# Optimization experiments

Hardware: AMD Instinct MI355X
Metric: run time of the kernel (lower is better)

The kernel has to match this reference:

```python
import jax, jax.numpy as jnp
import numpy as np

N = 50000      # nodes
E = 1_600_000  # edges
DIN, HID, OUT, H = 128, 32, 32, 4


def _glorot(key, shape):
    fan_in, fan_out = shape[0], shape[1] if len(shape) > 1 else shape[0]
    s = jnp.sqrt(6.0 / (fan_in + fan_out)).astype(jnp.float32)
    return jax.random.uniform(key, shape, jnp.float32, -s, s)


def setup_inputs() -> dict:
    key = jax.random.key(0)
    ks = jax.random.split(key, 16)
    inp = {
        "x": jax.random.normal(ks[0], (N, DIN), jnp.float32),
        "edge_index": jax.random.randint(ks[1], (2, E), 0, N, dtype=jnp.int32),
        "edge_weight": jax.random.uniform(ks[2], (E, 1), jnp.float32),
        # layer 1: in=DIN, heads=H, out=HID, concat=True
        "Wl1": _glorot(ks[3], (DIN, H * HID)),
        "Wr1": _glorot(ks[4], (DIN, H * HID)),
        "We1": _glorot(ks[5], (1, H * HID)),
        "att1": _glorot(ks[6], (H, HID)),
        "b1": jnp.zeros((H * HID,), jnp.float32),
        # layer 2: in=H*HID, heads=H, out=OUT, concat=False (mean over heads)
        "Wl2": _glorot(ks[7], (H * HID, H * OUT)),
        "Wr2": _glorot(ks[8], (H * HID, H * OUT)),
        "We2": _glorot(ks[9], (1, H * OUT)),
        "att2": _glorot(ks[10], (H, OUT)),
        "b2": jnp.zeros((OUT,), jnp.float32),
    }
    return inp


def gatv2_layer(x, edge_index, edge_weight, Wl, Wr, We, att, b, concat):
    """Faithful PyG GATv2Conv (share_weights=False, negative_slope=0.2,
    add_self_loops=True with fill_value='mean' for edge_attr)."""
    n = x.shape[0]
    heads, c = att.shape
    src, dst = edge_index[0], edge_index[1]
    # add self loops with mean edge weight (PyG default when edge_dim is set)
    loop = jnp.arange(n, dtype=edge_index.dtype)
    src = jnp.concatenate([src, loop])
    dst = jnp.concatenate([dst, loop])
    ew = jnp.concatenate(
        [edge_weight, jnp.full((n, edge_weight.shape[1]), jnp.mean(edge_weight), edge_weight.dtype)], axis=0)

    xl = (x @ Wl).reshape(n, heads, c)   # source transform (lin_l)
    xr = (x @ Wr).reshape(n, heads, c)   # target transform (lin_r)
    e_feat = (ew @ We).reshape(-1, heads, c)

    z = jax.nn.leaky_relu(xl[src] + xr[dst] + e_feat, 0.2)   # [E', H, C]
    logits = jnp.einsum('ehc,hc->eh', z, att)                # [E', H]

    # segment softmax over incoming edges of each target node
    m = jax.ops.segment_max(logits, dst, num_segments=n)
    m = jnp.where(jnp.isfinite(m), m, 0.0)
    p = jnp.exp(logits - m[dst])
    denom = jax.ops.segment_sum(p, dst, num_segments=n)
    alpha = p / (denom[dst] + 1e-16)                          # [E', H]

    out = jax.ops.segment_sum(xl[src] * alpha[..., None], dst, num_segments=n)  # [N, H, C]
    out = out.reshape(n, heads * c) if concat else out.mean(axis=1)
    return out + b


def reference(x, edge_index, edge_weight, Wl1, Wr1, We1, att1, b1,
              Wl2, Wr2, We2, att2, b2):
    h = gatv2_layer(x, edge_index, edge_weight, Wl1, Wr1, We1, att1, b1, concat=True)
    h = jax.nn.elu(h)
    out = gatv2_layer(h, edge_index, edge_weight, Wl2, Wr2, We2, att2, b2, concat=False)
    return out
```

## Files before the change

kernel.cpp:

```cpp
#include <hip/hip_runtime.h>
#include <hip/hip_fp16.h>
#include <math.h>


typedef _Float16 half8 __attribute__((ext_vector_type(8)));
typedef float floatx4 __attribute__((ext_vector_type(4)));

__global__ __launch_bounds__(256) void bucket_hist_sum(
    const int* __restrict__ dst, const float* __restrict__ ew,
    int* __restrict__ bcnt, float* __restrict__ sumbuf, int E) {
    __shared__ int h[256];
    h[threadIdx.x] = 0;
    __syncthreads();
    float s = 0.f;
    for (int i = blockIdx.x * blockDim.x + threadIdx.x; i < E; i += gridDim.x * blockDim.x) {
        atomicAdd(&h[dst[i] >> 8], 1);
        s += ew[i];
    }
#pragma unroll
    for (int off = 1; off <= 32; off <<= 1)
        s += __shfl_xor(s, off, 64);
    if ((threadIdx.x & 63) == 0)
        atomicAdd(sumbuf, s);
    __syncthreads();
    int v = h[threadIdx.x];
    if (v) atomicAdd(&bcnt[threadIdx.x], v);
}

__global__ void bucket_scan(const int* __restrict__ bcnt, int* __restrict__ bbase,
                            int* __restrict__ bcur, int NBK) {
    __shared__ int sh[256];
    int t = threadIdx.x;
    int v = (t < NBK) ? bcnt[t] : 0;
    sh[t] = v;
    __syncthreads();
    for (int off = 1; off < 256; off <<= 1) {
        int y = 0;
        if (t >= off) y = sh[t - off];
        __syncthreads();
        sh[t] += y;
        __syncthreads();
    }
    int ex = sh[t] - v;
    if (t <= NBK) bbase[t] = ex;
    if (t < NBK) bcur[t] = ex;
}

__global__ __launch_bounds__(256) void partition_kernel(
    const int* __restrict__ src, const int* __restrict__ dst, const float* __restrict__ ew,
    int* __restrict__ bcur, int2* __restrict__ srec, int E) {
    __shared__ int h[256];
    __shared__ int gb[256];
    const int t = threadIdx.x;
    h[t] = 0;
    __syncthreads();
    const int base = blockIdx.x * 4096;
    int d[16], sv[16];
    float wv[16];
#pragma unroll
    for (int j = 0; j < 16; j++) {
        int i = base + t + j * 256;
        if (i < E) {
            d[j] = dst[i];
            sv[j] = src[i];
            wv[j] = ew[i];
            atomicAdd(&h[d[j] >> 8], 1);
        } else {
            d[j] = -1;
        }
    }
    __syncthreads();
    int cntt = h[t];
    if (cntt) gb[t] = atomicAdd(&bcur[t], cntt);
    h[t] = 0;
    __syncthreads();
#pragma unroll
    for (int j = 0; j < 16; j++) {
        if (d[j] >= 0) {
            int b = d[j] >> 8;
            int r = atomicAdd(&h[b], 1);
            int pos = gb[b] + r;
            srec[pos] = make_int2(sv[j] | ((d[j] & 255) << 20), __float_as_int(wv[j]));
        }
    }
}

__global__ __launch_bounds__(256) void dst_hist_kernel(
    const int2* __restrict__ srec, const int* __restrict__ bbase,
    int* __restrict__ cnt, int N) {
    __shared__ int h[256];
    const int t = threadIdx.x;
    const int b = blockIdx.x;
    h[t] = 0;
    __syncthreads();
    const int e0 = bbase[b], e1 = bbase[b + 1];
    for (int i = e0 + t; i < e1; i += 256)
        atomicAdd(&h[(srec[i].x >> 20) & 255], 1);
    __syncthreads();
    int node = (b << 8) + t;
    if (node < N) cnt[node] = h[t];
}

__global__ void scan1_kernel(const int* __restrict__ cnt, int* __restrict__ rowp,
                             int* __restrict__ bsum, int N) {
    __shared__ int sh[256];
    int i = blockIdx.x * 256 + threadIdx.x;
    int v = (i < N) ? (cnt[i] + 1) : 0;
    sh[threadIdx.x] = v;
    __syncthreads();
    for (int off = 1; off < 256; off <<= 1) {
        int y = 0;
        if ((int)threadIdx.x >= off) y = sh[threadIdx.x - off];
        __syncthreads();
        sh[threadIdx.x] += y;
        __syncthreads();
    }
    int incl = sh[threadIdx.x];
    if (i < N) rowp[i] = incl - v;
    if (threadIdx.x == 255) bsum[blockIdx.x] = incl;
}

__global__ void scan2_kernel(int* __restrict__ bsum, int nb) {
    __shared__ int sh[256];
    int v = ((int)threadIdx.x < nb) ? bsum[threadIdx.x] : 0;
    sh[threadIdx.x] = v;
    __syncthreads();
    for (int off = 1; off < 256; off <<= 1) {
        int y = 0;
        if ((int)threadIdx.x >= off) y = sh[threadIdx.x - off];
        __syncthreads();
        sh[threadIdx.x] += y;
        __syncthreads();
    }
    int incl = sh[threadIdx.x];
    if ((int)threadIdx.x < nb) bsum[threadIdx.x] = incl - v;
}

__global__ void scan3_kernel(int* __restrict__ rowp, const int* __restrict__ bsum,
                             const int* __restrict__ cnt, const float* __restrict__ sumbuf,
                             int2* __restrict__ crec, int N, int E) {
    int i = blockIdx.x * 256 + threadIdx.x;
    if (i < N) {
        int rp = rowp[i] + bsum[blockIdx.x];
        rowp[i] = rp;
        crec[rp + cnt[i]] = make_int2(i, __float_as_int(sumbuf[0] * (1.0f / (float)E)));
    }
    if (i == 0) rowp[N] = E + N;
}

__global__ __launch_bounds__(256) void refine_kernel(
    const int2* __restrict__ srec, const int* __restrict__ bbase,
    const int* __restrict__ rowp, int2* __restrict__ crec, int N) {
    __shared__ int cur[256];
    const int t = threadIdx.x;
    const int b = blockIdx.x;
    int node = (b << 8) + t;
    cur[t] = (node < N) ? rowp[node] : 0;
    __syncthreads();
    const int e0 = bbase[b], e1 = bbase[b + 1];
    for (int i = e0 + t; i < e1; i += 256) {
        int2 rec = srec[i];
        int dlow = (rec.x >> 20) & 255;
        int pos = atomicAdd(&cur[dlow], 1);
        crec[pos] = make_int2(rec.x & 0xFFFFF, rec.y);
    }
}

__global__ __launch_bounds__(256) void prep_w_kernel(
    const float* __restrict__ Wa, const float* __restrict__ Wb,
    _Float16* __restrict__ Wh) {
    int tid = blockIdx.x * 256 + threadIdx.x;
    int j = tid & 7;
    int lane = (tid >> 3) & 63;
    int f = tid >> 9;
    int kk = f & 3;
    int ct = f >> 2;
    int col = ct * 16 + (lane & 15);
    int k = kk * 32 + ((lane >> 4) << 3) + j;
    float v = (col < 128) ? Wa[k * 128 + col] : Wb[k * 128 + (col - 128)];
    Wh[tid] = (_Float16)v;
}

__global__ __launch_bounds__(256) void gemm_mfma_kernel(
    const float* __restrict__ X, const _Float16* __restrict__ Wh,
    __half* __restrict__ Yh, float* __restrict__ Yb, int N) {
    __shared__ _Float16 Xs[64 * 128];
    const int tid = threadIdx.x;
    const int lane = tid & 63;
    const int w = tid >> 6;
    const int rb = blockIdx.x * 64;

    half8 wf[4][4];
#pragma unroll
    for (int ct = 0; ct < 4; ct++)
#pragma unroll
        for (int kk = 0; kk < 4; kk++)
            wf[ct][kk] = *(const half8*)(Wh + (size_t)(((w * 4 + ct) * 4 + kk) * 512 + lane * 8));

#pragma unroll
    for (int it = 0; it < 8; it++) {
        int c = it * 256 + tid;
        int row = c >> 5;
        int f4 = c & 31;
        float4 v = make_float4(0.f, 0.f, 0.f, 0.f);
        if (rb + row < N)
            v = ((const float4*)X)[(size_t)(rb + row) * 32 + f4];
        _Float16 h[4] = {(_Float16)v.x, (_Float16)v.y, (_Float16)v.z, (_Float16)v.w};
        int byteoff = row * 256 + ((f4 * 8) ^ ((row & 7) << 4));
        *(uint2*)((char*)Xs + byteoff) = *(uint2*)h;
    }
    __syncthreads();

    floatx4 acc[4][4];
#pragma unroll
    for (int ct = 0; ct < 4; ct++)
#pragma unroll
        for (int rt = 0; rt < 4; rt++)
            acc[ct][rt] = (floatx4){0.f, 0.f, 0.f, 0.f};

#pragma unroll
    for (int kk = 0; kk < 4; kk++) {
        half8 xf[4];
#pragma unroll
        for (int rt = 0; rt < 4; rt++) {
            int row = rt * 16 + (lane & 15);
            int kb = kk * 64 + ((lane >> 4) << 4);
            int off = row * 256 + (kb ^ ((row & 7) << 4));
            xf[rt] = *(const half8*)((const char*)Xs + off);
        }
#pragma unroll
        for (int ct = 0; ct < 4; ct++)
#pragma unroll
            for (int rt = 0; rt < 4; rt++)
                acc[ct][rt] = __builtin_amdgcn_mfma_f32_16x16x32_f16(
                    wf[ct][kk], xf[rt], acc[ct][rt], 0, 0, 0);
    }

    const int rsub = lane & 15;
    const int c4 = (lane >> 4) << 2;
#pragma unroll
    for (int ct = 0; ct < 4; ct++) {
        int gct = w * 4 + ct;
#pragma unroll
        for (int rt = 0; rt < 4; rt++) {
            int row = rb + rt * 16 + rsub;
            if (row < N) {
                floatx4 a = acc[ct][rt];
                if (gct < 8) {
                    int col = gct * 16 + c4;
                    __half2 hp[2];
                    hp[0] = __floats2half2_rn(a[0], a[1]);
                    hp[1] = __floats2half2_rn(a[2], a[3]);
                    *(uint2*)(Yh + (size_t)row * 128 + col) = *(uint2*)hp;
                } else {
                    int col = (gct - 8) * 16 + c4;
                    *(float4*)(Yb + (size_t)row * 128 + col) =
                        make_float4(a[0], a[1], a[2], a[3]);
                }
            }
        }
    }
}

template <int CTRL>
__device__ __forceinline__ float dpp_sum_step(float v) {
    int t = __builtin_amdgcn_update_dpp(0, __float_as_int(v), CTRL, 0xF, 0xF, true);
    return v + __int_as_float(t);
}

__device__ __forceinline__ float2 cvt_h2(unsigned u) {
    __half2 h = *(__half2*)&u;
    return __half22float2(h);
}

__global__ __launch_bounds__(256) void agg_kernel(
    const __half* __restrict__ xlh, const float* __restrict__ xr,
    const int* __restrict__ rowp, const int2* __restrict__ crec,
    const float* __restrict__ We, const float* __restrict__ att, const float* __restrict__ bias,
    float* __restrict__ out, int N, int mode) {
    const int wid = threadIdx.x >> 6;
    const int lane = threadIdx.x & 63;
    const int n = blockIdx.x * 4 + wid;
    if (n >= N) return;
    const int g = lane >> 4;
    const int q = lane & 15;
    const int c0 = q << 3;
    const float LOG2E = 1.4426950408889634f;

    float we[8], xv[8], at6[8], at4[8];
    {
        float4 wA = *(const float4*)(We + c0);
        float4 wB = *(const float4*)(We + c0 + 4);
        we[0]=wA.x; we[1]=wA.y; we[2]=wA.z; we[3]=wA.w;
        we[4]=wB.x; we[5]=wB.y; we[6]=wB.z; we[7]=wB.w;
        float4 rA = *(const float4*)(xr + (size_t)n * 128 + c0);
        float4 rB = *(const float4*)(xr + (size_t)n * 128 + c0 + 4);
        xv[0]=rA.x; xv[1]=rA.y; xv[2]=rA.z; xv[3]=rA.w;
        xv[4]=rB.x; xv[5]=rB.y; xv[6]=rB.z; xv[7]=rB.w;
        float4 aA = *(const float4*)(att + c0);
        float4 aB = *(const float4*)(att + c0 + 4);
        float av[8] = {aA.x, aA.y, aA.z, aA.w, aB.x, aB.y, aB.z, aB.w};
#pragma unroll
        for (int c = 0; c < 8; c++) {
            at6[c] = 0.6f * LOG2E * av[c];
            at4[c] = 0.4f * LOG2E * av[c];
        }
    }

    float acc[8];
#pragma unroll
    for (int c = 0; c < 8; c++) acc[c] = 0.f;
    float l0 = 0.f;

    const int e0 = __builtin_amdgcn_readfirstlane(rowp[n]);
    const int e1 = __builtin_amdgcn_readfirstlane(rowp[n + 1]);
    const int cnt = e1 - e0;
    const int T = (cnt + 3) >> 2;

    auto recload = [&](int i) -> int2 {
        int idx = e0 + (i << 2) + g;
        idx = (idx < e1 - 1) ? idx : (e1 - 1);
        return crec[idx];
    };
    auto gatherx = [&](int s) -> int4 {
        return *(const int4*)(xlh + (size_t)s * 128 + c0);
    };
    auto process = [&](int4 xh, float w, bool valid) {
        float2 x01 = cvt_h2(xh.x), x23 = cvt_h2(xh.y);
        float2 x45 = cvt_h2(xh.z), x67 = cvt_h2(xh.w);
        float xs[8] = {x01.x, x01.y, x23.x, x23.y, x45.x, x45.y, x67.x, x67.y};
        float p = 0.f;
#pragma unroll
        for (int c = 0; c < 8; c++) {
            float z = xs[c] + fmaf(w, we[c], xv[c]);
            p = fmaf(at6[c], z, fmaf(at4[c], fabsf(z), p));
        }
        p = dpp_sum_step<0xB1>(p);
        p = dpp_sum_step<0x4E>(p);
        float qe = valid ? __builtin_amdgcn_exp2f(p) : 0.f;
        l0 += qe;
#pragma unroll
        for (int c = 0; c < 8; c++) acc[c] = fmaf(qe, xs[c], acc[c]);
    };

    int2 r0 = recload(0), r1 = recload(1), r2 = recload(2), r3 = recload(3);
    int4 x0 = gatherx(r0.x), x1 = gatherx(r1.x);
    for (int i = 0; i < T; ++i) {
        int2 r4 = recload(i + 4);
        int4 x2 = gatherx(r2.x);
        process(x0, __int_as_float(r0.y), (e0 + (i << 2) + g) < e1);
        r0 = r1; r1 = r2; r2 = r3; r3 = r4;
        x0 = x1; x1 = x2;
    }

    l0 += __shfl_xor(l0, 16, 64);
    l0 += __shfl_xor(l0, 32, 64);
#pragma unroll
    for (int c = 0; c < 8; c++) {
        acc[c] += __shfl_xor(acc[c], 16, 64);
        acc[c] += __shfl_xor(acc[c], 32, 64);
    }
    float rdenom = 1.0f / (l0 + 1e-16f);
    float r[8];
#pragma unroll
    for (int c = 0; c < 8; c++) r[c] = acc[c] * rdenom;

    if (mode == 0) {
        if (g == 0) {
            float4 bA = *(const float4*)(bias + c0);
            float4 bB = *(const float4*)(bias + c0 + 4);
            float bv[8] = {bA.x, bA.y, bA.z, bA.w, bB.x, bB.y, bB.z, bB.w};
            float o[8];
#pragma unroll
            for (int c = 0; c < 8; c++) {
                float v = r[c] + bv[c];
                o[c] = (v > 0.f) ? v : (__expf(v) - 1.f);
            }
            float* op = out + (size_t)n * 128 + c0;
            *(float4*)op       = make_float4(o[0], o[1], o[2], o[3]);
            *(float4*)(op + 4) = make_float4(o[4], o[5], o[6], o[7]);
        }
    } else {
#pragma unroll
        for (int c = 0; c < 8; c++) {
            r[c] += __shfl_xor(r[c], 4, 64);
            r[c] += __shfl_xor(r[c], 8, 64);
        }
        if (lane < 4) {
            int w0 = lane << 3;
            float4 bA = *(const float4*)(bias + w0);
            float4 bB = *(const float4*)(bias + w0 + 4);
            float bv[8] = {bA.x, bA.y, bA.z, bA.w, bB.x, bB.y, bB.z, bB.w};
            float o[8];
#pragma unroll
            for (int c = 0; c < 8; c++) o[c] = 0.25f * r[c] + bv[c];
            float* op = out + (size_t)n * 32 + w0;
            *(float4*)op       = make_float4(o[0], o[1], o[2], o[3]);
            *(float4*)(op + 4) = make_float4(o[4], o[5], o[6], o[7]);
        }
    }
}

extern "C" void kernel_launch(void* const* d_in, const int* in_sizes, int n_in,
                              void* d_out, int out_size, void* d_ws, size_t ws_size,
                              hipStream_t stream) {
    const float* x    = (const float*)d_in[0];
    const int*  eidx  = (const int*)d_in[1];
    const float* ew   = (const float*)d_in[2];
    const float* Wl1  = (const float*)d_in[3];
    const float* Wr1  = (const float*)d_in[4];
    const float* We1  = (const float*)d_in[5];
    const float* att1 = (const float*)d_in[6];
    const float* b1   = (const float*)d_in[7];
    const float* Wl2  = (const float*)d_in[8];
    const float* Wr2  = (const float*)d_in[9];
    const float* We2  = (const float*)d_in[10];
    const float* att2 = (const float*)d_in[11];
    const float* b2   = (const float*)d_in[12];

    const int N = in_sizes[0] / 128;
    const int E = in_sizes[1] / 2;
    const int* src = eidx;
    const int* dst = eidx + E;
    const int NBK = (N + 255) >> 8;

    char* p = (char*)d_ws;
    auto alloc = [&](size_t bytes) -> void* {
        void* r = (void*)p;
        p += (bytes + 255) & ~(size_t)255;
        return r;
    };
    __half* xlh   = (__half*)alloc((size_t)N * 128 * sizeof(__half));
    float* xr     = (float*)alloc((size_t)N * 128 * sizeof(float));
    float* h1     = (float*)alloc((size_t)N * 128 * sizeof(float));
    int2*  crec   = (int2*)alloc((size_t)(E + N) * sizeof(int2));
    int*   rowp   = (int*)alloc((size_t)(N + 1) * sizeof(int));
    int*   cnt    = (int*)alloc((size_t)N * sizeof(int));
    int*   bcnt   = (int*)alloc(260 * sizeof(int));
    float* sumbuf = (float*)(bcnt + 256);
    int*   bbase  = (int*)alloc(260 * sizeof(int));
    int*   bcur   = (int*)alloc(260 * sizeof(int));
    int*   bsum   = (int*)alloc(256 * sizeof(int));
    _Float16* Wh1 = (_Float16*)alloc(32768 * sizeof(_Float16));
    _Float16* Wh2 = (_Float16*)alloc(32768 * sizeof(_Float16));
    int2*  srec   = (int2*)h1;

    hipMemsetAsync(bcnt, 0, 260 * sizeof(int), stream);

    prep_w_kernel<<<128, 256, 0, stream>>>(Wl1, Wr1, Wh1);
    prep_w_kernel<<<128, 256, 0, stream>>>(Wl2, Wr2, Wh2);

    bucket_hist_sum<<<1024, 256, 0, stream>>>(dst, ew, bcnt, sumbuf, E);
    bucket_scan<<<1, 256, 0, stream>>>(bcnt, bbase, bcur, NBK);
    partition_kernel<<<(E + 4095) / 4096, 256, 0, stream>>>(src, dst, ew, bcur, srec, E);
    dst_hist_kernel<<<NBK, 256, 0, stream>>>(srec, bbase, cnt, N);

    int nb = (N + 255) / 256;
    scan1_kernel<<<nb, 256, 0, stream>>>(cnt, rowp, bsum, N);
    scan2_kernel<<<1, 256, 0, stream>>>(bsum, nb);
    scan3_kernel<<<nb, 256, 0, stream>>>(rowp, bsum, cnt, sumbuf, crec, N, E);

    refine_kernel<<<NBK, 256, 0, stream>>>(srec, bbase, rowp, crec, N);

    gemm_mfma_kernel<<<(N + 63) / 64, 256, 0, stream>>>(x, Wh1, xlh, xr, N);
    agg_kernel<<<(N + 3) / 4, 256, 0, stream>>>(xlh, xr, rowp, crec,
                                                We1, att1, b1, h1, N, 0);
    gemm_mfma_kernel<<<(N + 63) / 64, 256, 0, stream>>>(h1, Wh2, xlh, xr, N);
    agg_kernel<<<(N + 3) / 4, 256, 0, stream>>>(xlh, xr, rowp, crec,
                                                We2, att2, b2, (float*)d_out, N, 1);
}
```

Before: 377.6 us.

## Replace two-pass bucket partition CSR build with direct global-atomic histogram and scatter

After: 499.8 us. 1.32x slower.

```diff
diff --git a/kernel.cpp b/kernel.cpp
--- a/kernel.cpp
+++ b/kernel.cpp
@@ -6,15 +6,12 @@
 typedef _Float16 half8 __attribute__((ext_vector_type(8)));
 typedef float floatx4 __attribute__((ext_vector_type(4)));
 
-__global__ __launch_bounds__(256) void bucket_hist_sum(
+__global__ __launch_bounds__(256) void hist_sum_kernel(
     const int* __restrict__ dst, const float* __restrict__ ew,
-    int* __restrict__ bcnt, float* __restrict__ sumbuf, int E) {
-    __shared__ int h[256];
-    h[threadIdx.x] = 0;
-    __syncthreads();
+    int* __restrict__ cnt, float* __restrict__ sumbuf, int E) {
     float s = 0.f;
-    for (int i = blockIdx.x * blockDim.x + threadIdx.x; i < E; i += gridDim.x * blockDim.x) {
-        atomicAdd(&h[dst[i] >> 8], 1);
+    for (int i = blockIdx.x * 256 + threadIdx.x; i < E; i += gridDim.x * 256) {
+        atomicAdd(&cnt[dst[i]], 1);
         s += ew[i];
     }
 #pragma unroll
@@ -22,83 +19,6 @@
         s += __shfl_xor(s, off, 64);
     if ((threadIdx.x & 63) == 0)
         atomicAdd(sumbuf, s);
-    __syncthreads();
-    int v = h[threadIdx.x];
-    if (v) atomicAdd(&bcnt[threadIdx.x], v);
-}
-
-__global__ void bucket_scan(const int* __restrict__ bcnt, int* __restrict__ bbase,
-                            int* __restrict__ bcur, int NBK) {
-    __shared__ int sh[256];
-    int t = threadIdx.x;
-    int v = (t < NBK) ? bcnt[t] : 0;
-    sh[t] = v;
-    __syncthreads();
-    for (int off = 1; off < 256; off <<= 1) {
-        int y = 0;
-        if (t >= off) y = sh[t - off];
-        __syncthreads();
-        sh[t] += y;
-        __syncthreads();
-    }
-    int ex = sh[t] - v;
-    if (t <= NBK) bbase[t] = ex;
-    if (t < NBK) bcur[t] = ex;
-}
-
-__global__ __launch_bounds__(256) void partition_kernel(
-    const int* __restrict__ src, const int* __restrict__ dst, const float* __restrict__ ew,
-    int* __restrict__ bcur, int2* __restrict__ srec, int E) {
-    __shared__ int h[256];
-    __shared__ int gb[256];
-    const int t = threadIdx.x;
-    h[t] = 0;
-    __syncthreads();
-    const int base = blockIdx.x * 4096;
-    int d[16], sv[16];
-    float wv[16];
-#pragma unroll
-    for (int j = 0; j < 16; j++) {
-        int i = base + t + j * 256;
-        if (i < E) {
-            d[j] = dst[i];
-            sv[j] = src[i];
-            wv[j] = ew[i];
-            atomicAdd(&h[d[j] >> 8], 1);
-        } else {
-            d[j] = -1;
-        }
-    }
-    __syncthreads();
-    int cntt = h[t];
-    if (cntt) gb[t] = atomicAdd(&bcur[t], cntt);
-    h[t] = 0;
-    __syncthreads();
-#pragma unroll
-    for (int j = 0; j < 16; j++) {
-        if (d[j] >= 0) {
-            int b = d[j] >> 8;
-            int r = atomicAdd(&h[b], 1);
-            int pos = gb[b] + r;
-            srec[pos] = make_int2(sv[j] | ((d[j] & 255) << 20), __float_as_int(wv[j]));
-        }
-    }
-}
-
-__global__ __launch_bounds__(256) void dst_hist_kernel(
-    const int2* __restrict__ srec, const int* __restrict__ bbase,
-    int* __restrict__ cnt, int N) {
-    __shared__ int h[256];
-    const int t = threadIdx.x;
-    const int b = blockIdx.x;
-    h[t] = 0;
-    __syncthreads();
-    const int e0 = bbase[b], e1 = bbase[b + 1];
-    for (int i = e0 + t; i < e1; i += 256)
-        atomicAdd(&h[(srec[i].x >> 20) & 255], 1);
-    __syncthreads();
-    int node = (b << 8) + t;
-    if (node < N) cnt[node] = h[t];
 }
 
 __global__ void scan1_kernel(const int* __restrict__ cnt, int* __restrict__ rowp,
@@ -138,31 +58,24 @@
 
 __global__ void scan3_kernel(int* __restrict__ rowp, const int* __restrict__ bsum,
                              const int* __restrict__ cnt, const float* __restrict__ sumbuf,
-                             int2* __restrict__ crec, int N, int E) {
+                             int2* __restrict__ crec, int* __restrict__ cur, int N, int E) {
     int i = blockIdx.x * 256 + threadIdx.x;
     if (i < N) {
         int rp = rowp[i] + bsum[blockIdx.x];
         rowp[i] = rp;
+        cur[i] = rp;
         crec[rp + cnt[i]] = make_int2(i, __float_as_int(sumbuf[0] * (1.0f / (float)E)));
     }
     if (i == 0) rowp[N] = E + N;
 }
 
-__global__ __launch_bounds__(256) void refine_kernel(
-    const int2* __restrict__ srec, const int* __restrict__ bbase,
-    const int* __restrict__ rowp, int2* __restrict__ crec, int N) {
-    __shared__ int cur[256];
-    const int t = threadIdx.x;
-    const int b = blockIdx.x;
-    int node = (b << 8) + t;
-    cur[t] = (node < N) ? rowp[node] : 0;
-    __syncthreads();
-    const int e0 = bbase[b], e1 = bbase[b + 1];
-    for (int i = e0 + t; i < e1; i += 256) {
-        int2 rec = srec[i];
-        int dlow = (rec.x >> 20) & 255;
-        int pos = atomicAdd(&cur[dlow], 1);
-        crec[pos] = make_int2(rec.x & 0xFFFFF, rec.y);
+__global__ __launch_bounds__(256) void scatter_kernel(
+    const int* __restrict__ src, const int* __restrict__ dst, const float* __restrict__ ew,
+    int* __restrict__ cur, int2* __restrict__ crec, int E) {
+    for (int i = blockIdx.x * 256 + threadIdx.x; i < E; i += gridDim.x * 256) {
+        int d = dst[i];
+        int pos = atomicAdd(&cur[d], 1);
+        crec[pos] = make_int2(src[i], __float_as_int(ew[i]));
     }
 }
 
@@ -422,7 +335,6 @@
     const int E = in_sizes[1] / 2;
     const int* src = eidx;
     const int* dst = eidx + E;
-    const int NBK = (N + 255) >> 8;
 
     char* p = (char*)d_ws;
     auto alloc = [&](size_t bytes) -> void* {
@@ -433,34 +345,29 @@
     __half* xlh   = (__half*)alloc((size_t)N * 128 * sizeof(__half));
     float* xr     = (float*)alloc((size_t)N * 128 * sizeof(float));
     float* h1     = (float*)alloc((size_t)N * 128 * sizeof(float));
-    int2*  crec   = (int2*)alloc((size_t)(E + N) * sizeof(int2));
+    int2*  crec   = (int2*)alloc((size_t)(E + N + 64) * sizeof(int2));
     int*   rowp   = (int*)alloc((size_t)(N + 1) * sizeof(int));
     int*   cnt    = (int*)alloc((size_t)N * sizeof(int));
-    int*   bcnt   = (int*)alloc(260 * sizeof(int));
-    float* sumbuf = (float*)(bcnt + 256);
-    int*   bbase  = (int*)alloc(260 * sizeof(int));
-    int*   bcur   = (int*)alloc(260 * sizeof(int));
+    int*   cur    = (int*)alloc((size_t)N * sizeof(int));
+    float* sumbuf = (float*)alloc(256);
     int*   bsum   = (int*)alloc(256 * sizeof(int));
     _Float16* Wh1 = (_Float16*)alloc(32768 * sizeof(_Float16));
     _Float16* Wh2 = (_Float16*)alloc(32768 * sizeof(_Float16));
-    int2*  srec   = (int2*)h1;
-
-    hipMemsetAsync(bcnt, 0, 260 * sizeof(int), stream);
+
+    hipMemsetAsync(cnt, 0, (size_t)N * sizeof(int), stream);
+    hipMemsetAsync(sumbuf, 0, 256, stream);
 
     prep_w_kernel<<<128, 256, 0, stream>>>(Wl1, Wr1, Wh1);
     prep_w_kernel<<<128, 256, 0, stream>>>(Wl2, Wr2, Wh2);
 
-    bucket_hist_sum<<<1024, 256, 0, stream>>>(dst, ew, bcnt, sumbuf, E);
-    bucket_scan<<<1, 256, 0, stream>>>(bcnt, bbase, bcur, NBK);
-    partition_kernel<<<(E + 4095) / 4096, 256, 0, stream>>>(src, dst, ew, bcur, srec, E);
-    dst_hist_kernel<<<NBK, 256, 0, stream>>>(srec, bbase, cnt, N);
+    hist_sum_kernel<<<1024, 256, 0, stream>>>(dst, ew, cnt, sumbuf, E);
 
     int nb = (N + 255) / 256;
     scan1_kernel<<<nb, 256, 0, stream>>>(cnt, rowp, bsum, N);
     scan2_kernel<<<1, 256, 0, stream>>>(bsum, nb);
-    scan3_kernel<<<nb, 256, 0, stream>>>(rowp, bsum, cnt, sumbuf, crec, N, E);
-
-    refine_kernel<<<NBK, 256, 0, stream>>>(srec, bbase, rowp, crec, N);
+    scan3_kernel<<<nb, 256, 0, stream>>>(rowp, bsum, cnt, sumbuf, crec, cur, N, E);
+
+    scatter_kernel<<<2048, 256, 0, stream>>>(src, dst, ew, cur, crec, E);
 
     gemm_mfma_kernel<<<(N + 63) / 64, 256, 0, stream>>>(x, Wh1, xlh, xr, N);
     agg_kernel<<<(N + 3) / 4, 256, 0, stream>>>(xlh, xr, rowp, crec,
```
